# Kernel tuning notes

Hardware: AMD Instinct MI355X
Metric: run time of the kernel (lower is better)

## Reference

```python
import jax, jax.numpy as jnp
import numpy as np

ND, B, L, D, V = 4, 128, 200, 512, 100002  # domains, batch, seqlen, hidden_units, item vocab (+2)
LN_EPS = 1e-8


def setup_inputs() -> dict:
    key = jax.random.key(0)
    ks = jax.random.split(key, 8)
    log_feats = jax.random.normal(ks[0], (ND, B, L, D), dtype=jnp.float32)  # per-domain encoder outputs
    lg_dom = jax.random.randint(ks[1], (B, ND, L), 0, 5)                    # domain labels in {0..4}, 0=pad
    pos_oth_dom = jax.random.randint(ks[2], (B, ND, L), 0, V)
    neg_oth_dom = jax.random.randint(ks[3], (B, ND, L), 0, V)
    # expert (per-domain) linear maps: nn.Linear(D, D) -> y = x @ W^T + b
    W_maps = jax.random.normal(ks[4], (ND, D, D), dtype=jnp.float32) / np.sqrt(D).astype(np.float32)
    b_maps = jnp.zeros((ND, D), dtype=jnp.float32)
    emb_table = jax.random.normal(ks[5], (V, D), dtype=jnp.float32) * 0.02  # domain_specific_item_emb
    ln_gamma = jnp.ones((D,), dtype=jnp.float32)
    ln_beta = jnp.zeros((D,), dtype=jnp.float32)
    return dict(log_feats=log_feats, W_maps=W_maps, b_maps=b_maps, emb_table=emb_table,
                ln_gamma=ln_gamma, ln_beta=ln_beta, lg_dom=lg_dom,
                pos_oth_dom=pos_oth_dom, neg_oth_dom=neg_oth_dom)


def reference(log_feats, W_maps, b_maps, emb_table, ln_gamma, ln_beta,
              lg_dom, pos_oth_dom, neg_oth_dom):
    # Dense MoE-style hard routing, exactly as the nested i,j loop in the source:
    # proj[i, j, b, l, e] = Linear_j(log_feats[i])  (nn.Linear: x @ W^T + b)
    proj = jnp.einsum('ibld,jed->ijble', log_feats, W_maps) + b_maps[None, :, None, None, :]
    lg = jnp.transpose(lg_dom, (1, 0, 2))  # [ND, B, L], per-domain token labels
    # mask[i, j, b, l] = (lg_dom[b, i, l] == j + 1); masks across j are disjoint
    mask = (lg[:, None, :, :] == (jnp.arange(ND) + 1)[None, :, None, None])
    routed = jnp.sum(proj * mask[..., None].astype(proj.dtype), axis=1)  # [ND, B, L, D]
    # emb_dropout is identity in eval mode; map_layernorm with eps=1e-8
    mu = routed.mean(-1, keepdims=True)
    var = ((routed - mu) ** 2).mean(-1, keepdims=True)
    mapped = (routed - mu) / jnp.sqrt(var + LN_EPS) * ln_gamma + ln_beta  # [ND, B, L, D]
    # cross-domain logits: (map_log_feats[i] * emb(pos/neg_oth_dom[:, i, :])).sum(-1)
    pos_emb = jnp.transpose(emb_table[pos_oth_dom], (1, 0, 2, 3))  # [ND, B, L, D]
    neg_emb = jnp.transpose(emb_table[neg_oth_dom], (1, 0, 2, 3))
    lg_pos_logits = jnp.sum(mapped * pos_emb, axis=-1)  # [ND, B, L]
    lg_neg_logits = jnp.sum(mapped * neg_emb, axis=-1)
    return mapped, lg_pos_logits, lg_neg_logits
```

## Files before the change

kernel.cpp:

```cpp
#include <hip/hip_runtime.h>

#define NDm 4
#define Bm 128
#define Lm 200
#define Dm 512
#define NT (NDm*Bm*Lm)
#define BM 32
#define NKB 16
#define LDA 40
#define MAPPED_ELEMS ((size_t)NT * Dm)

typedef __attribute__((ext_vector_type(8))) short bf16x8;
typedef __attribute__((ext_vector_type(4))) float f32x4;

__device__ __forceinline__ unsigned short f2bf(float f) {
  unsigned int u = __float_as_uint(f);
  u += 0x7fffu + ((u >> 16) & 1u);
  return (unsigned short)(u >> 16);
}

__global__ __launch_bounds__(256) void prep_kernel(const float* __restrict__ W,
                                                   unsigned short* __restrict__ wbf,
                                                   int* __restrict__ counts) {
  int idx = blockIdx.x * 256 + threadIdx.x;
  if (blockIdx.x == 0 && threadIdx.x < 8) counts[threadIdx.x] = 0;
  int k = idx & 511;
  int n = (idx >> 9) & 511;
  int j = idx >> 18;
  int kb = k >> 5, kk = k & 31;
  wbf[(((size_t)(j*NKB + kb))*Dm + n)*32 + kk] = f2bf(W[idx]);
}

__global__ __launch_bounds__(256) void route_kernel(const int* __restrict__ lg,
                                                    int* __restrict__ counts,
                                                    int* __restrict__ lists) {
  int tt = blockIdx.x * 256 + threadIdx.x;
  int i = tt / (Bm*Lm);
  int r = tt - i*(Bm*Lm);
  int b = r / Lm;
  int l = r - b*Lm;
  int lab = lg[(b*NDm + i)*Lm + l];
  int bucket = (lab >= 1) ? (lab - 1) : 4;
  int lane = threadIdx.x & 63;
  int slot = 0;
  #pragma unroll
  for (int v = 0; v < 5; ++v) {
    unsigned long long m = __ballot(bucket == v);
    if (m) {
      int leader = __ffsll((unsigned long long)m) - 1;
      int base = 0;
      if (lane == leader) base = atomicAdd(&counts[v], __popcll(m));
      base = __shfl(base, leader, 64);
      if (bucket == v)
        slot = base + __popcll(m & ((1ull << lane) - 1ull));
    }
  }
  lists[bucket*NT + slot] = tt;
}

__global__ __launch_bounds__(256) void moe_kernel(
    const float* __restrict__ logf, const float* __restrict__ bmaps,
    const float* __restrict__ emb, const float* __restrict__ gamma,
    const float* __restrict__ beta, const int* __restrict__ counts,
    const int* __restrict__ lists, const unsigned short* __restrict__ wbf,
    const int* __restrict__ posd, const int* __restrict__ negd,
    float* __restrict__ out) {
  __shared__ unsigned short Alds[BM * LDA];
  __shared__ unsigned short Wlds[Dm * LDA];
  __shared__ float reds[4][BM];
  __shared__ float redq[4][BM];
  __shared__ float mu_s[BM];
  __shared__ float rs_s[BM];
  __shared__ int tok_s[BM];
  __shared__ int pr_s[BM];
  __shared__ int nr_s[BM];

  const int e = blockIdx.y;
  const int cnt = counts[e];
  const int tile0 = blockIdx.x * BM;
  if (tile0 >= cnt) return;

  const int tid = threadIdx.x;
  const int wave = tid >> 6;
  const int lane = tid & 63;
  const int t = lane & 15;
  const int q = lane >> 4;

  if (tid < BM) {
    int idx = tile0 + tid;
    int tok = -1, pr = 0, nr = 0;
    if (idx < cnt) {
      tok = lists[e*NT + idx];
      int i = tok / (Bm*Lm);
      int r2 = tok - i*(Bm*Lm);
      int b = r2 / Lm;
      int l = r2 - b*Lm;
      int off = (b*NDm + i)*Lm + l;
      pr = posd[off];
      nr = negd[off];
    }
    tok_s[tid] = tok; pr_s[tid] = pr; nr_s[tid] = nr;
  }
  __syncthreads();

  f32x4 acc[2][8];
  #pragma unroll
  for (int mt = 0; mt < 2; ++mt)
    #pragma unroll
    for (int nt = 0; nt < 8; ++nt)
      acc[mt][nt] = (f32x4){0.f, 0.f, 0.f, 0.f};

  if (e < 4) {
    const int arow = tid >> 3;
    const int apart = tid & 7;
    const int atok = tok_s[arow];
    #pragma nounroll
    for (int kb = 0; kb < NKB; ++kb) {
      float4 av = make_float4(0.f, 0.f, 0.f, 0.f);
      if (atok >= 0)
        av = *(const float4*)(logf + (size_t)atok*Dm + kb*32 + apart*4);
      ushort4 ah;
      ah.x = f2bf(av.x); ah.y = f2bf(av.y); ah.z = f2bf(av.z); ah.w = f2bf(av.w);
      *(ushort4*)&Alds[arow*LDA + apart*4] = ah;
      const unsigned short* wsrc = wbf + ((size_t)(e*NKB + kb)) * (Dm*32);
      #pragma unroll
      for (int u = 0; u < 8; ++u) {
        int eidx = (u*256 + tid) * 8;
        int n = eidx >> 5;
        int kk = eidx & 31;
        uint4 d = *(const uint4*)(wsrc + eidx);
        *(uint4*)&Wlds[n*LDA + kk] = d;
      }
      __syncthreads();
      bf16x8 af[2];
      #pragma unroll
      for (int mt = 0; mt < 2; ++mt)
        af[mt] = *(const bf16x8*)&Alds[(mt*16 + t)*LDA + q*8];
      bf16x8 bfr[8];
      #pragma unroll
      for (int nt = 0; nt < 8; ++nt)
        bfr[nt] = *(const bf16x8*)&Wlds[(wave*128 + nt*16 + t)*LDA + q*8];
      #pragma unroll
      for (int mt = 0; mt < 2; ++mt)
        #pragma unroll
        for (int nt = 0; nt < 8; ++nt)
          acc[mt][nt] = __builtin_amdgcn_mfma_f32_16x16x32_bf16(af[mt], bfr[nt], acc[mt][nt], 0, 0, 0);
      __syncthreads();
    }
  }

  const int wbase = wave * 128;
  float g[8], bb[8], bi[8];
  #pragma unroll
  for (int nt = 0; nt < 8; ++nt) {
    int n = wbase + nt*16 + t;
    g[nt]  = gamma[n];
    bb[nt] = beta[n];
    bi[nt] = (e < 4) ? bmaps[e*Dm + n] : 0.f;
  }
  #pragma unroll
  for (int mt = 0; mt < 2; ++mt) {
    #pragma unroll
    for (int r = 0; r < 4; ++r) {
      float s = 0.f, s2 = 0.f;
      #pragma unroll
      for (int nt = 0; nt < 8; ++nt) {
        float v = acc[mt][nt][r] + bi[nt];
        acc[mt][nt][r] = v;
        s += v; s2 += v*v;
      }
      #pragma unroll
      for (int d = 1; d < 16; d <<= 1) {
        s  += __shfl_xor(s, d, 64);
        s2 += __shfl_xor(s2, d, 64);
      }
      if (t == 0) {
        int m = mt*16 + q*4 + r;
        reds[wave][m] = s;
        redq[wave][m] = s2;
      }
    }
  }
  __syncthreads();
  if (tid < BM) {
    float S  = reds[0][tid] + reds[1][tid] + reds[2][tid] + reds[3][tid];
    float S2 = redq[0][tid] + redq[1][tid] + redq[2][tid] + redq[3][tid];
    float mu = S * (1.f/Dm);
    float var = fmaxf(S2 * (1.f/Dm) - mu*mu, 0.f);
    mu_s[tid] = mu;
    rs_s[tid] = rsqrtf(var + 1e-8f);
  }
  __syncthreads();

  #pragma unroll
  for (int mt = 0; mt < 2; ++mt) {
    #pragma unroll
    for (int r = 0; r < 4; ++r) {
      int m = mt*16 + q*4 + r;
      float mu = mu_s[m];
      float rs = rs_s[m];
      int tok = tok_s[m];
      float pp = 0.f, nn = 0.f;
      if (tok >= 0) {
        const float* pe = emb + (size_t)pr_s[m]*Dm;
        const float* ne = emb + (size_t)nr_s[m]*Dm;
        float* od = out + (size_t)tok*Dm;
        #pragma unroll
        for (int nt = 0; nt < 8; ++nt) {
          int n = wbase + nt*16 + t;
          float val = (acc[mt][nt][r] - mu) * rs * g[nt] + bb[nt];
          od[n] = val;
          pp += val * pe[n];
          nn += val * ne[n];
        }
      }
      #pragma unroll
      for (int d = 1; d < 16; d <<= 1) {
        pp += __shfl_xor(pp, d, 64);
        nn += __shfl_xor(nn, d, 64);
      }
      if (t == 0) {
        reds[wave][m] = pp;
        redq[wave][m] = nn;
      }
    }
  }
  __syncthreads();
  if (tid < BM) {
    int tok = tok_s[tid];
    if (tok >= 0) {
      float P  = reds[0][tid] + reds[1][tid] + reds[2][tid] + reds[3][tid];
      float Nn = redq[0][tid] + redq[1][tid] + redq[2][tid] + redq[3][tid];
      out[MAPPED_ELEMS + tok] = P;
      out[MAPPED_ELEMS + NT + tok] = Nn;
    }
  }
}

extern "C" void kernel_launch(void* const* d_in, const int* in_sizes, int n_in,
                              void* d_out, int out_size, void* d_ws, size_t ws_size,
                              hipStream_t stream) {
  const float* logf  = (const float*)d_in[0];
  const float* Wm    = (const float*)d_in[1];
  const float* bm    = (const float*)d_in[2];
  const float* emb   = (const float*)d_in[3];
  const float* gamma = (const float*)d_in[4];
  const float* beta  = (const float*)d_in[5];
  const int*   lg    = (const int*)d_in[6];
  const int*   posd  = (const int*)d_in[7];
  const int*   negd  = (const int*)d_in[8];
  float* out = (float*)d_out;

  char* ws = (char*)d_ws;
  int* counts = (int*)ws;
  int* lists  = (int*)(ws + 128);
  unsigned short* wbf = (unsigned short*)(ws + 128 + (size_t)5*NT*4);

  prep_kernel<<<4096, 256, 0, stream>>>(Wm, wbf, counts);
  route_kernel<<<NT/256, 256, 0, stream>>>(lg, counts, lists);
  dim3 grid(NT/BM, 5);
  moe_kernel<<<grid, 256, 0, stream>>>(logf, bm, emb, gamma, beta,
                                       counts, lists, wbf, posd, negd, out);
}
```

Baseline: 719.0 us.

## Stage full A tile in LDS, stream W from global, coalesce epilogue via LDS

The whole 32x512 activation tile is converted to bf16 once and kept in LDS. Weight fragments are then read directly from global/L2 into registers, which removes the per-k-block W staging and the two barriers per iteration. The epilogue writes pre-norm values to LDS, 16 rows at a time. Each wave then handles whole rows with float4 loads and stores of the output and embeddings, replacing the scattered 4-byte accesses. Launch bounds request 3 blocks per CU. W is no longer shared through LDS, so each wave fetches its own B fragments from cache, and the extra row-major LDS buffer adds pressure.

New measurement: 671.7 us. 1.07x faster.

```diff
diff --git a/kernel.cpp b/kernel.cpp
--- a/kernel.cpp
+++ b/kernel.cpp
@@ -7,7 +7,8 @@
 #define NT (NDm*Bm*Lm)
 #define BM 32
 #define NKB 16
-#define LDA 40
+#define ASTR 520
+#define FSTR 516
 #define MAPPED_ELEMS ((size_t)NT * Dm)
 
 typedef __attribute__((ext_vector_type(8))) short bf16x8;
@@ -58,19 +59,20 @@
   lists[bucket*NT + slot] = tt;
 }
 
-__global__ __launch_bounds__(256) void moe_kernel(
+__global__ __launch_bounds__(256, 3) void moe_kernel(
     const float* __restrict__ logf, const float* __restrict__ bmaps,
     const float* __restrict__ emb, const float* __restrict__ gamma,
     const float* __restrict__ beta, const int* __restrict__ counts,
     const int* __restrict__ lists, const unsigned short* __restrict__ wbf,
     const int* __restrict__ posd, const int* __restrict__ negd,
     float* __restrict__ out) {
-  __shared__ unsigned short Alds[BM * LDA];
-  __shared__ unsigned short Wlds[Dm * LDA];
-  __shared__ float reds[4][BM];
-  __shared__ float redq[4][BM];
-  __shared__ float mu_s[BM];
-  __shared__ float rs_s[BM];
+  __shared__ __align__(16) unsigned char smem[BM * ASTR * 2];
+  unsigned short* Alds = (unsigned short*)smem;
+  float* Flds = (float*)smem;
+  __shared__ float reds[4][16];
+  __shared__ float redq[4][16];
+  __shared__ float mu_s[16];
+  __shared__ float rs_s[16];
   __shared__ int tok_s[BM];
   __shared__ int pr_s[BM];
   __shared__ int nr_s[BM];
@@ -112,61 +114,59 @@
 
   if (e < 4) {
     const int arow = tid >> 3;
-    const int apart = tid & 7;
+    const int acol0 = (tid & 7) * 4;
     const int atok = tok_s[arow];
-    #pragma nounroll
-    for (int kb = 0; kb < NKB; ++kb) {
+    const float* ap = logf + (size_t)(atok < 0 ? 0 : atok) * Dm;
+    #pragma unroll 4
+    for (int it = 0; it < 16; ++it) {
+      int col = acol0 + it * 32;
       float4 av = make_float4(0.f, 0.f, 0.f, 0.f);
-      if (atok >= 0)
-        av = *(const float4*)(logf + (size_t)atok*Dm + kb*32 + apart*4);
+      if (atok >= 0) av = *(const float4*)(ap + col);
       ushort4 ah;
       ah.x = f2bf(av.x); ah.y = f2bf(av.y); ah.z = f2bf(av.z); ah.w = f2bf(av.w);
-      *(ushort4*)&Alds[arow*LDA + apart*4] = ah;
-      const unsigned short* wsrc = wbf + ((size_t)(e*NKB + kb)) * (Dm*32);
+      *(ushort4*)&Alds[arow*ASTR + col] = ah;
+    }
+    __syncthreads();
+
+    const unsigned short* pB = wbf + (size_t)e*(NKB*Dm*32)
+                                   + (size_t)(wave*128 + t)*32 + q*8;
+    const unsigned short* pA0 = &Alds[t*ASTR + q*8];
+    #pragma unroll 2
+    for (int kb = 0; kb < NKB; ++kb) {
+      bf16x8 a0 = *(const bf16x8*)(pA0 + kb*32);
+      bf16x8 a1 = *(const bf16x8*)(pA0 + 16*ASTR + kb*32);
       #pragma unroll
-      for (int u = 0; u < 8; ++u) {
-        int eidx = (u*256 + tid) * 8;
-        int n = eidx >> 5;
-        int kk = eidx & 31;
-        uint4 d = *(const uint4*)(wsrc + eidx);
-        *(uint4*)&Wlds[n*LDA + kk] = d;
-      }
-      __syncthreads();
-      bf16x8 af[2];
-      #pragma unroll
-      for (int mt = 0; mt < 2; ++mt)
-        af[mt] = *(const bf16x8*)&Alds[(mt*16 + t)*LDA + q*8];
-      bf16x8 bfr[8];
-      #pragma unroll
-      for (int nt = 0; nt < 8; ++nt)
-        bfr[nt] = *(const bf16x8*)&Wlds[(wave*128 + nt*16 + t)*LDA + q*8];
-      #pragma unroll
-      for (int mt = 0; mt < 2; ++mt)
-        #pragma unroll
-        for (int nt = 0; nt < 8; ++nt)
-          acc[mt][nt] = __builtin_amdgcn_mfma_f32_16x16x32_bf16(af[mt], bfr[nt], acc[mt][nt], 0, 0, 0);
-      __syncthreads();
-    }
-  }
-
-  const int wbase = wave * 128;
-  float g[8], bb[8], bi[8];
-  #pragma unroll
-  for (int nt = 0; nt < 8; ++nt) {
-    int n = wbase + nt*16 + t;
-    g[nt]  = gamma[n];
-    bb[nt] = beta[n];
-    bi[nt] = (e < 4) ? bmaps[e*Dm + n] : 0.f;
-  }
+      for (int nt = 0; nt < 8; ++nt) {
+        bf16x8 b = *(const bf16x8*)(pB + kb*(Dm*32) + nt*512);
+        acc[0][nt] = __builtin_amdgcn_mfma_f32_16x16x32_bf16(a0, b, acc[0][nt], 0, 0, 0);
+        acc[1][nt] = __builtin_amdgcn_mfma_f32_16x16x32_bf16(a1, b, acc[1][nt], 0, 0, 0);
+      }
+    }
+  }
+  __syncthreads();
+
+  float bi[8];
+  #pragma unroll
+  for (int nt = 0; nt < 8; ++nt)
+    bi[nt] = (e < 4) ? bmaps[e*Dm + wave*128 + nt*16 + t] : 0.f;
+  float4 gm[2], bt[2];
+  #pragma unroll
+  for (int c = 0; c < 2; ++c) {
+    int col = c*256 + lane*4;
+    gm[c] = *(const float4*)(gamma + col);
+    bt[c] = *(const float4*)(beta + col);
+  }
+
   #pragma unroll
   for (int mt = 0; mt < 2; ++mt) {
     #pragma unroll
     for (int r = 0; r < 4; ++r) {
+      int row16 = q*4 + r;
       float s = 0.f, s2 = 0.f;
       #pragma unroll
       for (int nt = 0; nt < 8; ++nt) {
         float v = acc[mt][nt][r] + bi[nt];
-        acc[mt][nt][r] = v;
+        Flds[row16*FSTR + wave*128 + nt*16 + t] = v;
         s += v; s2 += v*v;
       }
       #pragma unroll
@@ -174,66 +174,57 @@
         s  += __shfl_xor(s, d, 64);
         s2 += __shfl_xor(s2, d, 64);
       }
-      if (t == 0) {
-        int m = mt*16 + q*4 + r;
-        reds[wave][m] = s;
-        redq[wave][m] = s2;
-      }
-    }
-  }
-  __syncthreads();
-  if (tid < BM) {
-    float S  = reds[0][tid] + reds[1][tid] + reds[2][tid] + reds[3][tid];
-    float S2 = redq[0][tid] + redq[1][tid] + redq[2][tid] + redq[3][tid];
-    float mu = S * (1.f/Dm);
-    float var = fmaxf(S2 * (1.f/Dm) - mu*mu, 0.f);
-    mu_s[tid] = mu;
-    rs_s[tid] = rsqrtf(var + 1e-8f);
-  }
-  __syncthreads();
-
-  #pragma unroll
-  for (int mt = 0; mt < 2; ++mt) {
+      if (t == 0) { reds[wave][row16] = s; redq[wave][row16] = s2; }
+    }
+    __syncthreads();
+    if (tid < 16) {
+      float S  = reds[0][tid] + reds[1][tid] + reds[2][tid] + reds[3][tid];
+      float S2 = redq[0][tid] + redq[1][tid] + redq[2][tid] + redq[3][tid];
+      float mu = S * (1.f/Dm);
+      float var = fmaxf(S2 * (1.f/Dm) - mu*mu, 0.f);
+      mu_s[tid] = mu;
+      rs_s[tid] = rsqrtf(var + 1e-8f);
+    }
+    __syncthreads();
     #pragma unroll
-    for (int r = 0; r < 4; ++r) {
-      int m = mt*16 + q*4 + r;
-      float mu = mu_s[m];
-      float rs = rs_s[m];
+    for (int rr = 0; rr < 4; ++rr) {
+      int row16 = wave*4 + rr;
+      int m = mt*16 + row16;
       int tok = tok_s[m];
-      float pp = 0.f, nn = 0.f;
       if (tok >= 0) {
+        float mu = mu_s[row16];
+        float rs = rs_s[row16];
         const float* pe = emb + (size_t)pr_s[m]*Dm;
         const float* ne = emb + (size_t)nr_s[m]*Dm;
         float* od = out + (size_t)tok*Dm;
+        float pp = 0.f, nn = 0.f;
         #pragma unroll
-        for (int nt = 0; nt < 8; ++nt) {
-          int n = wbase + nt*16 + t;
-          float val = (acc[mt][nt][r] - mu) * rs * g[nt] + bb[nt];
-          od[n] = val;
-          pp += val * pe[n];
-          nn += val * ne[n];
+        for (int c = 0; c < 2; ++c) {
+          int col = c*256 + lane*4;
+          float4 v  = *(const float4*)&Flds[row16*FSTR + col];
+          float4 p4 = *(const float4*)(pe + col);
+          float4 n4 = *(const float4*)(ne + col);
+          float4 o;
+          o.x = (v.x - mu)*rs*gm[c].x + bt[c].x;
+          o.y = (v.y - mu)*rs*gm[c].y + bt[c].y;
+          o.z = (v.z - mu)*rs*gm[c].z + bt[c].z;
+          o.w = (v.w - mu)*rs*gm[c].w + bt[c].w;
+          *(float4*)(od + col) = o;
+          pp += o.x*p4.x + o.y*p4.y + o.z*p4.z + o.w*p4.w;
+          nn += o.x*n4.x + o.y*n4.y + o.z*n4.z + o.w*n4.w;
         }
-      }
-      #pragma unroll
-      for (int d = 1; d < 16; d <<= 1) {
-        pp += __shfl_xor(pp, d, 64);
-        nn += __shfl_xor(nn, d, 64);
-      }
-      if (t == 0) {
-        reds[wave][m] = pp;
-        redq[wave][m] = nn;
-      }
-    }
-  }
-  __syncthreads();
-  if (tid < BM) {
-    int tok = tok_s[tid];
-    if (tok >= 0) {
-      float P  = reds[0][tid] + reds[1][tid] + reds[2][tid] + reds[3][tid];
-      float Nn = redq[0][tid] + redq[1][tid] + redq[2][tid] + redq[3][tid];
-      out[MAPPED_ELEMS + tok] = P;
-      out[MAPPED_ELEMS + NT + tok] = Nn;
-    }
+        #pragma unroll
+        for (int d = 1; d < 64; d <<= 1) {
+          pp += __shfl_xor(pp, d, 64);
+          nn += __shfl_xor(nn, d, 64);
+        }
+        if (lane == 0) {
+          out[MAPPED_ELEMS + tok] = pp;
+          out[MAPPED_ELEMS + NT + tok] = nn;
+        }
+      }
+    }
+    __syncthreads();
   }
 }
 
```
